# Performance work log

Measured on AMD Instinct MI355X. Metric: run time of the kernel, lower is better.

Reference implementation:

```python
import jax, jax.numpy as jnp
import numpy as np
import math

D_MODEL = 1024
HEADS = 16
HEAD_DIM = D_MODEL // HEADS
B, S = 2, 2048


def setup_inputs() -> dict:
    key = jax.random.key(0)
    ks = jax.random.split(key, 7)
    scale = 1.0 / math.sqrt(D_MODEL)
    return {
        "query": jax.random.normal(ks[0], (B, S, D_MODEL), dtype=jnp.float32),
        "key": jax.random.normal(ks[1], (B, S, D_MODEL), dtype=jnp.float32),
        "value": jax.random.normal(ks[2], (B, S, D_MODEL), dtype=jnp.float32),
        # causal mask, broadcast over batch and heads: [1, 1, S, S]
        "mask": jnp.tril(jnp.ones((S, S), dtype=bool))[None, None],
        "Wq": jax.random.normal(ks[3], (D_MODEL, D_MODEL), dtype=jnp.float32) * scale,
        "Wk": jax.random.normal(ks[4], (D_MODEL, D_MODEL), dtype=jnp.float32) * scale,
        "Wv": jax.random.normal(ks[5], (D_MODEL, D_MODEL), dtype=jnp.float32) * scale,
        "Wo": jax.random.normal(ks[6], (D_MODEL, D_MODEL), dtype=jnp.float32) * scale,
    }


def reference(query, key, value, mask, Wq, Wk, Wv, Wo):
    # bias-free projections (nn.Linear: x @ W.T)
    q = query @ Wq.T  # [B, S, D]
    k = key @ Wk.T
    v = value @ Wv.T

    def split_heads(x):  # [B, S, D] -> [B, H, S, Dh]
        return x.reshape(B, -1, HEADS, HEAD_DIM).transpose(0, 2, 1, 3)

    q, k, v = split_heads(q), split_heads(k), split_heads(v)

    # scores: [B, H, S, S]
    scores = jnp.einsum("bhsd,bhtd->bhst", q, k) / math.sqrt(HEAD_DIM)
    scores = jnp.where(mask, scores, -1e9)
    attn = jax.nn.softmax(scores, axis=-1)
    # dropout omitted (eval-mode reference; p=0.1 in training)
    out = jnp.einsum("bhst,bhtd->bhsd", attn, v)  # [B, H, S, Dh]
    out = out.transpose(0, 2, 1, 3).reshape(B, -1, D_MODEL)
    return out @ Wo.T
```

## Files before the change

kernel.cpp:

```cpp
#include <hip/hip_runtime.h>

#define BATCH 2
#define SEQ   2048
#define DMODEL 1024
#define NHEADS 16
#define HDIM  64

typedef __attribute__((ext_vector_type(8))) short short8v;
typedef __attribute__((ext_vector_type(4))) float f32x4;
typedef unsigned int uint32;

__device__ __forceinline__ unsigned short bf16rne(float x) {
    uint32 u = __float_as_uint(x);
    return (unsigned short)((u + 0x7FFFu + ((u >> 16) & 1u)) >> 16);
}
__device__ __forceinline__ void split1(float x, unsigned short& h, unsigned short& l) {
    uint32 u = __float_as_uint(x);
    uint32 hb = (u + 0x7FFFu + ((u >> 16) & 1u)) & 0xFFFF0000u;
    h = (unsigned short)(hb >> 16);
    float r = x - __uint_as_float(hb);
    l = bf16rne(r);
}

__global__ __launch_bounds__(256)
void cvt_hi3(const float* __restrict__ s0, const float* __restrict__ s1,
             const float* __restrict__ s2, short* __restrict__ d0,
             short* __restrict__ d1, short* __restrict__ d2, int n) {
    const float* src; short* dst;
    if (blockIdx.y == 0)      { src = s0; dst = d0; }
    else if (blockIdx.y == 1) { src = s1; dst = d1; }
    else                      { src = s2; dst = d2; }
    int i = (blockIdx.x * 256 + threadIdx.x) * 4;
    if (i >= n) return;
    float4 x = *reinterpret_cast<const float4*>(src + i);
    *reinterpret_cast<ushort4*>(dst + i) =
        make_ushort4(bf16rne(x.x), bf16rne(x.y), bf16rne(x.z), bf16rne(x.w));
}

__global__ __launch_bounds__(256)
void split_hl(const float* __restrict__ src, short* __restrict__ hi,
              short* __restrict__ lo, int n) {
    int i = (blockIdx.x * 256 + threadIdx.x) * 4;
    if (i >= n) return;
    float4 x = *reinterpret_cast<const float4*>(src + i);
    unsigned short h0, h1, h2, h3, l0, l1, l2, l3;
    split1(x.x, h0, l0); split1(x.y, h1, l1);
    split1(x.z, h2, l2); split1(x.w, h3, l3);
    *reinterpret_cast<ushort4*>(hi + i) = make_ushort4(h0, h1, h2, h3);
    *reinterpret_cast<ushort4*>(lo + i) = make_ushort4(l0, l1, l2, l3);
}

__device__ __forceinline__ void gload_lds16(const void* g, void* l) {
    __builtin_amdgcn_global_load_lds((const __attribute__((address_space(1))) void*)g,
                                     (__attribute__((address_space(3))) void*)l,
                                     16, 0, 0);
}

__global__ __launch_bounds__(256)
void gemm_qkv_bf16(const short* __restrict__ aq, const short* __restrict__ ak,
                   const short* __restrict__ av,
                   const short* __restrict__ wq, const short* __restrict__ wk,
                   const short* __restrict__ wv,
                   short* __restrict__ qo, short* __restrict__ ko,
                   short* __restrict__ vo) {
    __shared__ short As[128 * 64];
    __shared__ short Bs[128 * 64];
    const int tid = threadIdx.x;
    const int lane = tid & 63;
    const int w = tid >> 6, wm = w >> 1, wn = w & 1;
    const int r = lane & 15, g = lane >> 4;

    int soff[4];
    #pragma unroll
    for (int c = 0; c < 4; ++c) {
        const int u = c * 256 + tid, row = u >> 3, s = u & 7;
        soff[c] = row * 1024 + ((s ^ (row & 7)) * 8);
    }

    const int z = blockIdx.z;
    const short* A; const short* B; int bm, bn;
    if (z == 0)      { A = aq; B = wq; bm = blockIdx.y * 128; bn = blockIdx.x * 128; }
    else if (z == 1) { A = ak; B = wk; bm = blockIdx.y * 128; bn = blockIdx.x * 128; }
    else             { A = wv; B = av; bm = blockIdx.x * 128; bn = blockIdx.y * 128; }

    f32x4 acc[4][4];
    #pragma unroll
    for (int i = 0; i < 4; ++i)
        #pragma unroll
        for (int j = 0; j < 4; ++j) acc[i][j] = (f32x4){0.f, 0.f, 0.f, 0.f};

    const short* Arow = A + (size_t)bm * 1024;
    const short* Brow = B + (size_t)bn * 1024;
    for (int k0 = 0; k0 < 1024; k0 += 64) {
        __syncthreads();
        #pragma unroll
        for (int c = 0; c < 4; ++c) {
            gload_lds16(Arow + k0 + soff[c], &As[(c * 256 + tid) * 8]);
            gload_lds16(Brow + k0 + soff[c], &Bs[(c * 256 + tid) * 8]);
        }
        __syncthreads();
        #pragma unroll
        for (int kk = 0; kk < 2; ++kk) {
            short8v af[4], bf[4];
            #pragma unroll
            for (int fm = 0; fm < 4; ++fm)
                af[fm] = *(const short8v*)&As[(wm * 64 + fm * 16 + r) * 64 +
                                              (((kk * 4 + g) ^ (r & 7))) * 8];
            #pragma unroll
            for (int fn = 0; fn < 4; ++fn)
                bf[fn] = *(const short8v*)&Bs[(wn * 64 + fn * 16 + r) * 64 +
                                              (((kk * 4 + g) ^ (r & 7))) * 8];
            #pragma unroll
            for (int fm = 0; fm < 4; ++fm)
                #pragma unroll
                for (int fn = 0; fn < 4; ++fn)
                    acc[fm][fn] = __builtin_amdgcn_mfma_f32_16x16x32_bf16(
                        af[fm], bf[fn], acc[fm][fn], 0, 0, 0);
        }
    }

    #pragma unroll
    for (int fm = 0; fm < 4; ++fm)
        #pragma unroll
        for (int fn = 0; fn < 4; ++fn)
            #pragma unroll
            for (int qi = 0; qi < 4; ++qi) {
                const int mrow = bm + wm * 64 + fm * 16 + g * 4 + qi;
                const int ncol = bn + wn * 64 + fn * 16 + r;
                const float v = acc[fm][fn][qi];
                if (z == 0) {
                    size_t idx = ((size_t)((mrow >> 11) * 16 + (ncol >> 6))) * (SEQ * 64)
                               + (size_t)(mrow & 2047) * 64 + (ncol & 63);
                    qo[idx] = (short)bf16rne(v * 0.125f);
                } else if (z == 1) {
                    size_t idx = ((size_t)((mrow >> 11) * 16 + (ncol >> 6))) * (SEQ * 64)
                               + (size_t)(mrow & 2047) * 64 + (ncol & 63);
                    ko[idx] = (short)bf16rne(v);
                } else {
                    size_t idx = ((size_t)((ncol >> 11) * 16 + (mrow >> 6))) * (SEQ * 64)
                               + (size_t)(mrow & 63) * SEQ + (ncol & 2047);
                    vo[idx] = (short)bf16rne(v);
                }
            }
}

__device__ __forceinline__ void gemm512_pass(const short* __restrict__ Arow,
                                             const short* __restrict__ Brow,
                                             short* As, short* Bs,
                                             f32x4 (&acc)[4][2], int tid) {
    const int lane = tid & 63;
    const int w = tid >> 6, wm = w >> 2, wn = w & 3;
    const int r = lane & 15, g = lane >> 4;
    int soff[2];
    #pragma unroll
    for (int c = 0; c < 2; ++c) {
        const int u = c * 512 + tid, row = u >> 3, s = u & 7;
        soff[c] = row * 1024 + ((s ^ (row & 7)) * 8);
    }
    for (int k0 = 0; k0 < 1024; k0 += 64) {
        __syncthreads();
        #pragma unroll
        for (int c = 0; c < 2; ++c) {
            gload_lds16(Arow + k0 + soff[c], &As[(c * 512 + tid) * 8]);
            gload_lds16(Brow + k0 + soff[c], &Bs[(c * 512 + tid) * 8]);
        }
        __syncthreads();
        #pragma unroll
        for (int kk = 0; kk < 2; ++kk) {
            short8v af[4], bf[2];
            #pragma unroll
            for (int fm = 0; fm < 4; ++fm)
                af[fm] = *(const short8v*)&As[(wm * 64 + fm * 16 + r) * 64 +
                                              (((kk * 4 + g) ^ (r & 7))) * 8];
            #pragma unroll
            for (int fn = 0; fn < 2; ++fn)
                bf[fn] = *(const short8v*)&Bs[(wn * 32 + fn * 16 + r) * 64 +
                                              (((kk * 4 + g) ^ (r & 7))) * 8];
            #pragma unroll
            for (int fm = 0; fm < 4; ++fm)
                #pragma unroll
                for (int fn = 0; fn < 2; ++fn)
                    acc[fm][fn] = __builtin_amdgcn_mfma_f32_16x16x32_bf16(
                        af[fm], bf[fn], acc[fm][fn], 0, 0, 0);
        }
    }
}

__global__ __launch_bounds__(512)
void gemm_out_f32(const short* __restrict__ Ah, const short* __restrict__ Al,
                  const short* __restrict__ Bh, const short* __restrict__ Bl,
                  float* __restrict__ C) {
    __shared__ short As[128 * 64];
    __shared__ short Bs[128 * 64];
    const int tid = threadIdx.x;
    const int bm = blockIdx.y * 128, bn = blockIdx.x * 128;

    f32x4 acc[4][2];
    #pragma unroll
    for (int i = 0; i < 4; ++i)
        #pragma unroll
        for (int j = 0; j < 2; ++j) acc[i][j] = (f32x4){0.f, 0.f, 0.f, 0.f};

    gemm512_pass(Ah + (size_t)bm * 1024, Bh + (size_t)bn * 1024, As, Bs, acc, tid);
    gemm512_pass(Ah + (size_t)bm * 1024, Bl + (size_t)bn * 1024, As, Bs, acc, tid);
    gemm512_pass(Al + (size_t)bm * 1024, Bh + (size_t)bn * 1024, As, Bs, acc, tid);

    const int lane = tid & 63;
    const int w = tid >> 6, wm = w >> 2, wn = w & 3;
    const int r = lane & 15, g = lane >> 4;
    #pragma unroll
    for (int fm = 0; fm < 4; ++fm)
        #pragma unroll
        for (int fn = 0; fn < 2; ++fn)
            #pragma unroll
            for (int qi = 0; qi < 4; ++qi) {
                const int mrow = bm + wm * 64 + fm * 16 + g * 4 + qi;
                const int ncol = bn + wn * 32 + fn * 16 + r;
                C[(size_t)mrow * DMODEL + ncol] = acc[fm][fn][qi];
            }
}

__global__ __launch_bounds__(256)
void attn_wave(const short* __restrict__ qh, const short* __restrict__ kh,
               const short* __restrict__ vt, short* __restrict__ oh,
               short* __restrict__ ol) {
    __shared__ short Pl[4][16 * 64];
    const int tid  = threadIdx.x;
    const int lane = tid & 63;
    const int wid  = tid >> 6;
    const int r = lane & 15;
    const int g = lane >> 4;
    const int w  = blockIdx.x * 4 + wid;
    const int bh = w & 31;
    const int c1 = w >> 5;
    short* Pw = Pl[wid];

    const short* qB = qh + (size_t)bh * SEQ * 64;
    const short* kB = kh + (size_t)bh * SEQ * 64;
    const short* vB = vt + (size_t)bh * 64 * SEQ;
    const int b = bh >> 4, h = bh & 15;

    #pragma unroll
    for (int half = 0; half < 2; ++half) {
        const int c  = half ? (127 - c1) : c1;
        const int nt = (c + 4) >> 2;

        short8v qf[2];
        #pragma unroll
        for (int kk = 0; kk < 2; ++kk)
            qf[kk] = *(const short8v*)(qB + (size_t)(c * 16 + r) * 64 + (kk * 4 + g) * 8);

        f32x4 oacc[4];
        #pragma unroll
        for (int fd = 0; fd < 4; ++fd) oacc[fd] = (f32x4){0.f, 0.f, 0.f, 0.f};
        float lsum[4] = {0.f, 0.f, 0.f, 0.f};

        for (int kt = 0; kt < nt; ++kt) {
            f32x4 sacc[4];
            #pragma unroll
            for (int fn = 0; fn < 4; ++fn) sacc[fn] = (f32x4){0.f, 0.f, 0.f, 0.f};
            #pragma unroll
            for (int kk = 0; kk < 2; ++kk) {
                short8v kf[4];
                #pragma unroll
                for (int fn = 0; fn < 4; ++fn)
                    kf[fn] = *(const short8v*)(kB +
                        (size_t)(kt * 64 + fn * 16 + r) * 64 + (kk * 4 + g) * 8);
                #pragma unroll
                for (int fn = 0; fn < 4; ++fn)
                    sacc[fn] = __builtin_amdgcn_mfma_f32_16x16x32_bf16(
                        qf[kk], kf[fn], sacc[fn], 0, 0, 0);
            }

            if (kt == nt - 1) {
                #pragma unroll
                for (int fn = 0; fn < 4; ++fn)
                    #pragma unroll
                    for (int qi = 0; qi < 4; ++qi) {
                        const int qg = c * 16 + g * 4 + qi;
                        const int kg = kt * 64 + fn * 16 + r;
                        if (kg > qg) sacc[fn][qi] = -1.0e30f;
                    }
            }

            #pragma unroll
            for (int fn = 0; fn < 4; ++fn)
                #pragma unroll
                for (int qi = 0; qi < 4; ++qi) {
                    const float p = __expf(sacc[fn][qi]);
                    sacc[fn][qi] = p;
                    lsum[qi] += p;
                }

            #pragma unroll
            for (int fn = 0; fn < 4; ++fn)
                #pragma unroll
                for (int qi = 0; qi < 4; ++qi) {
                    const int ql = g * 4 + qi;
                    const int kl = fn * 16 + r;
                    Pw[ql * 64 + (((kl >> 3) ^ (ql & 7)) << 3) + (kl & 7)] =
                        (short)bf16rne(sacc[fn][qi]);
                }

            #pragma unroll
            for (int kk = 0; kk < 2; ++kk) {
                short8v pf = *(const short8v*)&Pw[r * 64 +
                                                  (((kk * 4 + g) ^ (r & 7))) * 8];
                short8v vf[4];
                #pragma unroll
                for (int fd = 0; fd < 4; ++fd)
                    vf[fd] = *(const short8v*)(vB + (size_t)(fd * 16 + r) * SEQ +
                                               kt * 64 + (kk * 4 + g) * 8);
                #pragma unroll
                for (int fd = 0; fd < 4; ++fd)
                    oacc[fd] = __builtin_amdgcn_mfma_f32_16x16x32_bf16(
                        pf, vf[fd], oacc[fd], 0, 0, 0);
            }
        }

        #pragma unroll
        for (int qi = 0; qi < 4; ++qi) {
            float s = lsum[qi];
            s += __shfl_xor(s, 1);
            s += __shfl_xor(s, 2);
            s += __shfl_xor(s, 4);
            s += __shfl_xor(s, 8);
            lsum[qi] = 1.0f / s;
        }

        #pragma unroll
        for (int fd = 0; fd < 4; ++fd)
            #pragma unroll
            for (int qi = 0; qi < 4; ++qi) {
                const float v = oacc[fd][qi] * lsum[qi];
                unsigned short hh, ll;
                split1(v, hh, ll);
                const int mg = b * SEQ + c * 16 + g * 4 + qi;
                const int nc = h * 64 + fd * 16 + r;
                const size_t idx = (size_t)mg * DMODEL + nc;
                oh[idx] = (short)hh; ol[idx] = (short)ll;
            }
    }
}

extern "C" void kernel_launch(void* const* d_in, const int* in_sizes, int n_in,
                              void* d_out, int out_size, void* d_ws, size_t ws_size,
                              hipStream_t stream) {
    const float* query = (const float*)d_in[0];
    const float* key   = (const float*)d_in[1];
    const float* value = (const float*)d_in[2];
    const float* Wq = (const float*)d_in[4];
    const float* Wk = (const float*)d_in[5];
    const float* Wv = (const float*)d_in[6];
    const float* Wo = (const float*)d_in[7];
    float* out = (float*)d_out;

    const size_t SD = (size_t)BATCH * SEQ * DMODEL;
    const size_t DD = (size_t)DMODEL * DMODEL;
    const int M = BATCH * SEQ;

    short* ws  = (short*)d_ws;
    short* aq  = ws;
    short* ak  = aq + SD;
    short* av  = ak + SD;
    short* wqh = av + SD;
    short* wkh = wqh + DD;
    short* wvh = wkh + DD;
    short* qh_ = wvh + DD;
    short* kh_ = qh_ + SD;
    short* vt_ = kh_ + SD;
    short* woh = vt_ + SD;
    short* wol = woh + DD;
    short* oh_ = aq;
    short* ol_ = ak;

    dim3 gc_a((unsigned)(SD / 1024), 3);
    cvt_hi3<<<gc_a, 256, 0, stream>>>(query, key, value, aq, ak, av, (int)SD);
    dim3 gc_w((unsigned)(DD / 1024), 3);
    cvt_hi3<<<gc_w, 256, 0, stream>>>(Wq, Wk, Wv, wqh, wkh, wvh, (int)DD);

    dim3 gq(DMODEL / 128, M / 128, 3);
    gemm_qkv_bf16<<<gq, 256, 0, stream>>>(aq, ak, av, wqh, wkh, wvh, qh_, kh_, vt_);

    attn_wave<<<512, 256, 0, stream>>>(qh_, kh_, vt_, oh_, ol_);

    split_hl<<<(int)(DD / 1024), 256, 0, stream>>>(Wo, woh, wol, (int)DD);

    dim3 go(DMODEL / 128, M / 128);
    gemm_out_f32<<<go, 512, 0, stream>>>(oh_, ol_, woh, wol, out);
}
```

Before: 341.2 us.

## Split attention KV loop across waves per 32-row query block with LDS reduction

Replaces the one-wave-per-16-query-rows attention kernel with a block-per-32-query-rows kernel whose four waves stride over the key tiles and then reduce partial outputs and row sums through shared memory. Each wave now processes two query fragments per K/V load, which doubles reuse of the K and V fragments, and the grid is ordered heaviest-first. In exchange it adds several block barriers and an LDS reduction epilogue, and the waves get uneven key-tile counts for short causal rows. The softmax still runs without a running max, as it did before.

```diff
diff --git a/kernel.cpp b/kernel.cpp
--- a/kernel.cpp
+++ b/kernel.cpp
@@ -220,126 +220,209 @@
             }
 }
 
-__global__ __launch_bounds__(256)
-void attn_wave(const short* __restrict__ qh, const short* __restrict__ kh,
-               const short* __restrict__ vt, short* __restrict__ oh,
-               short* __restrict__ ol) {
-    __shared__ short Pl[4][16 * 64];
+__global__ __launch_bounds__(256, 3)
+void attn_split(const short* __restrict__ qh, const short* __restrict__ kh,
+                const short* __restrict__ vt, short* __restrict__ oh,
+                short* __restrict__ ol) {
+    __shared__ short Pl[4][32 * 64];
+    __shared__ float Ls[4][32];
     const int tid  = threadIdx.x;
     const int lane = tid & 63;
     const int wid  = tid >> 6;
     const int r = lane & 15;
     const int g = lane >> 4;
-    const int w  = blockIdx.x * 4 + wid;
-    const int bh = w & 31;
-    const int c1 = w >> 5;
+    const int c  = 63 - (int)blockIdx.x;
+    const int bh = blockIdx.y;
     short* Pw = Pl[wid];
+    float* Ob = reinterpret_cast<float*>(&Pl[0][0]);
 
     const short* qB = qh + (size_t)bh * SEQ * 64;
     const short* kB = kh + (size_t)bh * SEQ * 64;
     const short* vB = vt + (size_t)bh * 64 * SEQ;
     const int b = bh >> 4, h = bh & 15;
-
-    #pragma unroll
-    for (int half = 0; half < 2; ++half) {
-        const int c  = half ? (127 - c1) : c1;
-        const int nt = (c + 4) >> 2;
-
-        short8v qf[2];
+    const int q0 = c * 32;
+    const int nt = (c + 2) >> 1;
+
+    short8v qf[2][2];
+    #pragma unroll
+    for (int fm = 0; fm < 2; ++fm)
         #pragma unroll
         for (int kk = 0; kk < 2; ++kk)
-            qf[kk] = *(const short8v*)(qB + (size_t)(c * 16 + r) * 64 + (kk * 4 + g) * 8);
-
-        f32x4 oacc[4];
-        #pragma unroll
-        for (int fd = 0; fd < 4; ++fd) oacc[fd] = (f32x4){0.f, 0.f, 0.f, 0.f};
-        float lsum[4] = {0.f, 0.f, 0.f, 0.f};
-
-        for (int kt = 0; kt < nt; ++kt) {
-            f32x4 sacc[4];
-            #pragma unroll
-            for (int fn = 0; fn < 4; ++fn) sacc[fn] = (f32x4){0.f, 0.f, 0.f, 0.f};
-            #pragma unroll
-            for (int kk = 0; kk < 2; ++kk) {
-                short8v kf[4];
+            qf[fm][kk] = *(const short8v*)(qB + (size_t)(q0 + fm * 16 + r) * 64 +
+                                           (kk * 4 + g) * 8);
+
+    f32x4 oacc[2][4];
+    float lsum[2][4];
+    #pragma unroll
+    for (int fm = 0; fm < 2; ++fm) {
+        #pragma unroll
+        for (int fd = 0; fd < 4; ++fd) oacc[fm][fd] = (f32x4){0.f, 0.f, 0.f, 0.f};
+        #pragma unroll
+        for (int qi = 0; qi < 4; ++qi) lsum[fm][qi] = 0.f;
+    }
+
+    for (int kt = wid; kt < nt; kt += 4) {
+        f32x4 sacc[2][4];
+        #pragma unroll
+        for (int fm = 0; fm < 2; ++fm)
+            #pragma unroll
+            for (int fn = 0; fn < 4; ++fn) sacc[fm][fn] = (f32x4){0.f, 0.f, 0.f, 0.f};
+        #pragma unroll
+        for (int kk = 0; kk < 2; ++kk) {
+            short8v kf[4];
+            #pragma unroll
+            for (int fn = 0; fn < 4; ++fn)
+                kf[fn] = *(const short8v*)(kB + (size_t)(kt * 64 + fn * 16 + r) * 64 +
+                                           (kk * 4 + g) * 8);
+            #pragma unroll
+            for (int fm = 0; fm < 2; ++fm)
                 #pragma unroll
                 for (int fn = 0; fn < 4; ++fn)
-                    kf[fn] = *(const short8v*)(kB +
-                        (size_t)(kt * 64 + fn * 16 + r) * 64 + (kk * 4 + g) * 8);
-                #pragma unroll
-                for (int fn = 0; fn < 4; ++fn)
-                    sacc[fn] = __builtin_amdgcn_mfma_f32_16x16x32_bf16(
-                        qf[kk], kf[fn], sacc[fn], 0, 0, 0);
-            }
-
-            if (kt == nt - 1) {
+                    sacc[fm][fn] = __builtin_amdgcn_mfma_f32_16x16x32_bf16(
+                        qf[fm][kk], kf[fn], sacc[fm][fn], 0, 0, 0);
+        }
+
+        if (kt == nt - 1) {
+            #pragma unroll
+            for (int fm = 0; fm < 2; ++fm)
                 #pragma unroll
                 for (int fn = 0; fn < 4; ++fn)
                     #pragma unroll
                     for (int qi = 0; qi < 4; ++qi) {
-                        const int qg = c * 16 + g * 4 + qi;
+                        const int qg = q0 + fm * 16 + g * 4 + qi;
                         const int kg = kt * 64 + fn * 16 + r;
-                        if (kg > qg) sacc[fn][qi] = -1.0e30f;
+                        if (kg > qg) sacc[fm][fn][qi] = -1.0e30f;
                     }
-            }
-
+        }
+
+        #pragma unroll
+        for (int fm = 0; fm < 2; ++fm)
             #pragma unroll
             for (int fn = 0; fn < 4; ++fn)
                 #pragma unroll
                 for (int qi = 0; qi < 4; ++qi) {
-                    const float p = __expf(sacc[fn][qi]);
-                    sacc[fn][qi] = p;
-                    lsum[qi] += p;
+                    const float p = __expf(sacc[fm][fn][qi]);
+                    sacc[fm][fn][qi] = p;
+                    lsum[fm][qi] += p;
                 }
 
+        #pragma unroll
+        for (int fm = 0; fm < 2; ++fm)
             #pragma unroll
             for (int fn = 0; fn < 4; ++fn)
                 #pragma unroll
                 for (int qi = 0; qi < 4; ++qi) {
-                    const int ql = g * 4 + qi;
+                    const int ql = fm * 16 + g * 4 + qi;
                     const int kl = fn * 16 + r;
                     Pw[ql * 64 + (((kl >> 3) ^ (ql & 7)) << 3) + (kl & 7)] =
-                        (short)bf16rne(sacc[fn][qi]);
+                        (short)bf16rne(sacc[fm][fn][qi]);
                 }
 
-            #pragma unroll
-            for (int kk = 0; kk < 2; ++kk) {
-                short8v pf = *(const short8v*)&Pw[r * 64 +
-                                                  (((kk * 4 + g) ^ (r & 7))) * 8];
-                short8v vf[4];
+        #pragma unroll
+        for (int kk = 0; kk < 2; ++kk) {
+            short8v pf[2], vf[4];
+            #pragma unroll
+            for (int fm = 0; fm < 2; ++fm)
+                pf[fm] = *(const short8v*)&Pw[(fm * 16 + r) * 64 +
+                                              (((kk * 4 + g) ^ (r & 7))) * 8];
+            #pragma unroll
+            for (int fd = 0; fd < 4; ++fd)
+                vf[fd] = *(const short8v*)(vB + (size_t)(fd * 16 + r) * SEQ +
+                                           kt * 64 + (kk * 4 + g) * 8);
+            #pragma unroll
+            for (int fm = 0; fm < 2; ++fm)
                 #pragma unroll
                 for (int fd = 0; fd < 4; ++fd)
-                    vf[fd] = *(const short8v*)(vB + (size_t)(fd * 16 + r) * SEQ +
-                                               kt * 64 + (kk * 4 + g) * 8);
-                #pragma unroll
-                for (int fd = 0; fd < 4; ++fd)
-                    oacc[fd] = __builtin_amdgcn_mfma_f32_16x16x32_bf16(
-                        pf, vf[fd], oacc[fd], 0, 0, 0);
-            }
-        }
-
+                    oacc[fm][fd] = __builtin_amdgcn_mfma_f32_16x16x32_bf16(
+                        pf[fm], vf[fd], oacc[fm][fd], 0, 0, 0);
+        }
+    }
+
+    #pragma unroll
+    for (int fm = 0; fm < 2; ++fm)
         #pragma unroll
         for (int qi = 0; qi < 4; ++qi) {
-            float s = lsum[qi];
+            float s = lsum[fm][qi];
             s += __shfl_xor(s, 1);
             s += __shfl_xor(s, 2);
             s += __shfl_xor(s, 4);
             s += __shfl_xor(s, 8);
-            lsum[qi] = 1.0f / s;
-        }
-
-        #pragma unroll
-        for (int fd = 0; fd < 4; ++fd)
+            lsum[fm][qi] = s;
+        }
+    if (r == 0) {
+        #pragma unroll
+        for (int fm = 0; fm < 2; ++fm)
+            #pragma unroll
+            for (int qi = 0; qi < 4; ++qi)
+                Ls[wid][fm * 16 + g * 4 + qi] = lsum[fm][qi];
+    }
+
+    __syncthreads();
+
+    if (wid >= 2) {
+        float* dst = Ob + (wid - 2) * 2048;
+        #pragma unroll
+        for (int fm = 0; fm < 2; ++fm)
+            #pragma unroll
+            for (int fd = 0; fd < 4; ++fd)
+                #pragma unroll
+                for (int qi = 0; qi < 4; ++qi)
+                    dst[(fm * 16 + g * 4 + qi) * 64 + fd * 16 + r] = oacc[fm][fd][qi];
+    }
+    __syncthreads();
+    if (wid < 2) {
+        const float* src = Ob + wid * 2048;
+        #pragma unroll
+        for (int fm = 0; fm < 2; ++fm)
+            #pragma unroll
+            for (int fd = 0; fd < 4; ++fd)
+                #pragma unroll
+                for (int qi = 0; qi < 4; ++qi)
+                    oacc[fm][fd][qi] += src[(fm * 16 + g * 4 + qi) * 64 + fd * 16 + r];
+    }
+    __syncthreads();
+    if (wid == 1) {
+        #pragma unroll
+        for (int fm = 0; fm < 2; ++fm)
+            #pragma unroll
+            for (int fd = 0; fd < 4; ++fd)
+                #pragma unroll
+                for (int qi = 0; qi < 4; ++qi)
+                    Ob[(fm * 16 + g * 4 + qi) * 64 + fd * 16 + r] = oacc[fm][fd][qi];
+    }
+    __syncthreads();
+    if (wid == 0) {
+        #pragma unroll
+        for (int fm = 0; fm < 2; ++fm)
+            #pragma unroll
+            for (int fd = 0; fd < 4; ++fd)
+                #pragma unroll
+                for (int qi = 0; qi < 4; ++qi)
+                    oacc[fm][fd][qi] += Ob[(fm * 16 + g * 4 + qi) * 64 + fd * 16 + r];
+
+        float inv[2][4];
+        #pragma unroll
+        for (int fm = 0; fm < 2; ++fm)
             #pragma unroll
             for (int qi = 0; qi < 4; ++qi) {
-                const float v = oacc[fd][qi] * lsum[qi];
-                unsigned short hh, ll;
-                split1(v, hh, ll);
-                const int mg = b * SEQ + c * 16 + g * 4 + qi;
-                const int nc = h * 64 + fd * 16 + r;
-                const size_t idx = (size_t)mg * DMODEL + nc;
-                oh[idx] = (short)hh; ol[idx] = (short)ll;
+                const int row = fm * 16 + g * 4 + qi;
+                inv[fm][qi] = 1.0f / (Ls[0][row] + Ls[1][row] + Ls[2][row] + Ls[3][row]);
             }
+
+        #pragma unroll
+        for (int fm = 0; fm < 2; ++fm)
+            #pragma unroll
+            for (int fd = 0; fd < 4; ++fd)
+                #pragma unroll
+                for (int qi = 0; qi < 4; ++qi) {
+                    const float v = oacc[fm][fd][qi] * inv[fm][qi];
+                    unsigned short hh, ll;
+                    split1(v, hh, ll);
+                    const int mg = b * SEQ + q0 + fm * 16 + g * 4 + qi;
+                    const int nc = h * 64 + fd * 16 + r;
+                    const size_t idx = (size_t)mg * DMODEL + nc;
+                    oh[idx] = (short)hh; ol[idx] = (short)ll;
+                }
     }
 }
 
@@ -382,7 +465,8 @@
     dim3 gq(DMODEL / 128, M / 128, 3);
     gemm_qkv_bf16<<<gq, 256, 0, stream>>>(aq, ak, av, wqh, wkh, wvh, qh_, kh_, vt_);
 
-    attn_wave<<<512, 256, 0, stream>>>(qh_, kh_, vt_, oh_, ol_);
+    dim3 ga(64, BATCH * NHEADS);
+    attn_split<<<ga, 256, 0, stream>>>(qh_, kh_, vt_, oh_, ol_);
 
     split_hl<<<(int)(DD / 1024), 256, 0, stream>>>(Wo, woh, wol, (int)DD);
 
```

After: 329.4 us. 1.04x faster.

## Prefetch next K tile and hoist V loads in attention, use exp2

Applied to the files above, without the earlier changes.

The attention kernel now double-buffers K fragments in registers, loading the next tile's K while the current tile is processed. It also issues the V loads before softmax so their latency overlaps with exp and LDS work. The Q scale folds in log2(e), so softmax can use the hardware exp2 directly instead of __expf. It adds launch bounds with min 2 blocks per SM, which raises register pressure and risks spills.

```diff
diff --git a/kernel.cpp b/kernel.cpp
--- a/kernel.cpp
+++ b/kernel.cpp
@@ -20,6 +20,13 @@
     h = (unsigned short)(hb >> 16);
     float r = x - __uint_as_float(hb);
     l = bf16rne(r);
+}
+__device__ __forceinline__ float fexp2(float x) {
+#if __has_builtin(__builtin_amdgcn_exp2f)
+    return __builtin_amdgcn_exp2f(x);
+#else
+    return exp2f(x);
+#endif
 }
 
 __global__ __launch_bounds__(256)
@@ -131,7 +138,7 @@
                 if (z == 0) {
                     size_t idx = ((size_t)((mrow >> 11) * 16 + (ncol >> 6))) * (SEQ * 64)
                                + (size_t)(mrow & 2047) * 64 + (ncol & 63);
-                    qo[idx] = (short)bf16rne(v * 0.125f);
+                    qo[idx] = (short)bf16rne(v * 0.18033688011112043f);
                 } else if (z == 1) {
                     size_t idx = ((size_t)((mrow >> 11) * 16 + (ncol >> 6))) * (SEQ * 64)
                                + (size_t)(mrow & 2047) * 64 + (ncol & 63);
@@ -220,10 +227,10 @@
             }
 }
 
-__global__ __launch_bounds__(256)
-void attn_wave(const short* __restrict__ qh, const short* __restrict__ kh,
-               const short* __restrict__ vt, short* __restrict__ oh,
-               short* __restrict__ ol) {
+__global__ __launch_bounds__(256, 2)
+void attn_wave_pf(const short* __restrict__ qh, const short* __restrict__ kh,
+                  const short* __restrict__ vt, short* __restrict__ oh,
+                  short* __restrict__ ol) {
     __shared__ short Pl[4][16 * 64];
     const int tid  = threadIdx.x;
     const int lane = tid & 63;
@@ -255,21 +262,35 @@
         for (int fd = 0; fd < 4; ++fd) oacc[fd] = (f32x4){0.f, 0.f, 0.f, 0.f};
         float lsum[4] = {0.f, 0.f, 0.f, 0.f};
 
-        for (int kt = 0; kt < nt; ++kt) {
+        short8v kfA[2][4], kfB[2][4];
+
+        auto tile_step = [&](short8v (&kcur)[2][4], short8v (&knxt)[2][4],
+                             int kt) __attribute__((always_inline)) {
             f32x4 sacc[4];
             #pragma unroll
             for (int fn = 0; fn < 4; ++fn) sacc[fn] = (f32x4){0.f, 0.f, 0.f, 0.f};
             #pragma unroll
-            for (int kk = 0; kk < 2; ++kk) {
-                short8v kf[4];
-                #pragma unroll
-                for (int fn = 0; fn < 4; ++fn)
-                    kf[fn] = *(const short8v*)(kB +
-                        (size_t)(kt * 64 + fn * 16 + r) * 64 + (kk * 4 + g) * 8);
+            for (int kk = 0; kk < 2; ++kk)
                 #pragma unroll
                 for (int fn = 0; fn < 4; ++fn)
                     sacc[fn] = __builtin_amdgcn_mfma_f32_16x16x32_bf16(
-                        qf[kk], kf[fn], sacc[fn], 0, 0, 0);
+                        qf[kk], kcur[kk][fn], sacc[fn], 0, 0, 0);
+
+            short8v vf[2][4];
+            #pragma unroll
+            for (int kk = 0; kk < 2; ++kk)
+                #pragma unroll
+                for (int fd = 0; fd < 4; ++fd)
+                    vf[kk][fd] = *(const short8v*)(vB + (size_t)(fd * 16 + r) * SEQ +
+                                                   kt * 64 + (kk * 4 + g) * 8);
+
+            if (kt + 1 < nt) {
+                #pragma unroll
+                for (int kk = 0; kk < 2; ++kk)
+                    #pragma unroll
+                    for (int fn = 0; fn < 4; ++fn)
+                        knxt[kk][fn] = *(const short8v*)(kB +
+                            (size_t)((kt + 1) * 64 + fn * 16 + r) * 64 + (kk * 4 + g) * 8);
             }
 
             if (kt == nt - 1) {
@@ -287,7 +308,7 @@
             for (int fn = 0; fn < 4; ++fn)
                 #pragma unroll
                 for (int qi = 0; qi < 4; ++qi) {
-                    const float p = __expf(sacc[fn][qi]);
+                    const float p = fexp2(sacc[fn][qi]);
                     sacc[fn][qi] = p;
                     lsum[qi] += p;
                 }
@@ -306,16 +327,26 @@
             for (int kk = 0; kk < 2; ++kk) {
                 short8v pf = *(const short8v*)&Pw[r * 64 +
                                                   (((kk * 4 + g) ^ (r & 7))) * 8];
-                short8v vf[4];
-                #pragma unroll
-                for (int fd = 0; fd < 4; ++fd)
-                    vf[fd] = *(const short8v*)(vB + (size_t)(fd * 16 + r) * SEQ +
-                                               kt * 64 + (kk * 4 + g) * 8);
                 #pragma unroll
                 for (int fd = 0; fd < 4; ++fd)
                     oacc[fd] = __builtin_amdgcn_mfma_f32_16x16x32_bf16(
-                        pf, vf[fd], oacc[fd], 0, 0, 0);
-            }
+                        pf, vf[kk][fd], oacc[fd], 0, 0, 0);
+            }
+        };
+
+        #pragma unroll
+        for (int kk = 0; kk < 2; ++kk)
+            #pragma unroll
+            for (int fn = 0; fn < 4; ++fn)
+                kfA[kk][fn] = *(const short8v*)(kB +
+                    (size_t)(fn * 16 + r) * 64 + (kk * 4 + g) * 8);
+
+        int kt = 0;
+        while (true) {
+            tile_step(kfA, kfB, kt);
+            ++kt; if (kt >= nt) break;
+            tile_step(kfB, kfA, kt);
+            ++kt; if (kt >= nt) break;
         }
 
         #pragma unroll
@@ -382,7 +413,7 @@
     dim3 gq(DMODEL / 128, M / 128, 3);
     gemm_qkv_bf16<<<gq, 256, 0, stream>>>(aq, ak, av, wqh, wkh, wvh, qh_, kh_, vt_);
 
-    attn_wave<<<512, 256, 0, stream>>>(qh_, kh_, vt_, oh_, ol_);
+    attn_wave_pf<<<512, 256, 0, stream>>>(qh_, kh_, vt_, oh_, ol_);
 
     split_hl<<<(int)(DD / 1024), 256, 0, stream>>>(Wo, woh, wol, (int)DD);
 
```

New measurement: 340.3 us. No clear change (-0.3%).
